# Optimization experiments

Hardware: AMD Instinct MI355X
Metric: run time of the kernel (lower is better)

## Reference

```python
import jax, jax.numpy as jnp
import numpy as np

TOP_K = 2
INIT_STD = 0.02
B, T, D, E, I = 2, 2048, 1024, 8, 512


def setup_inputs() -> dict:
    key = jax.random.key(0)
    k0, k1, k2, k3, k4 = jax.random.split(key, 5)
    return {
        "x": jax.random.normal(k0, (B, T, D), dtype=jnp.float32),
        "router_w": (jax.random.normal(k1, (E, D), dtype=jnp.float32) * INIT_STD),
        "w_gate": (jax.random.normal(k2, (E, I, D), dtype=jnp.float32) * INIT_STD),
        "w_up": (jax.random.normal(k3, (E, I, D), dtype=jnp.float32) * INIT_STD),
        "w_down": (jax.random.normal(k4, (E, D, I), dtype=jnp.float32) * INIT_STD),
    }


def _moe_forward(x, router_w, w_gate, w_up, w_down):
    # x: [B, T, D]; router_w: [E, D]; w_gate/w_up: [E, I, D]; w_down: [E, D, I]
    b, t, d = x.shape
    e = router_w.shape[0]
    gate_logits = jnp.einsum('btd,ed->bte', x, router_w)          # [B, T, E]
    top_w, sel = jax.lax.top_k(gate_logits, TOP_K)                # [B, T, K]
    probs = jax.nn.softmax(top_w, axis=-1)                        # softmax over selected experts only

    n = b * t
    xf = x.reshape(n, d)                                          # [N, D]
    sel_f = sel.reshape(n, TOP_K)
    probs_f = probs.reshape(n, TOP_K)
    # combine weights per (token, expert); zero for unselected experts
    gates = jnp.zeros((n, e), dtype=x.dtype).at[
        jnp.arange(n)[:, None], sel_f].add(probs_f)               # [N, E]

    # SwiGLU expert FFN (no bias). Gated-dense formulation: unselected experts
    # have gate weight exactly 0, so this is bit-for-bit the same math as
    # dispatch + grouped GEMM + combine. scan over experts keeps memory at
    # one [N, I] intermediate at a time.
    def body(acc, ws):
        wg, wu, wd, g = ws                                        # [I,D],[I,D],[D,I],[N]
        h = jax.nn.silu(xf @ wg.T) * (xf @ wu.T)                  # [N, I]
        return acc + g[:, None] * (h @ wd.T), None

    out, _ = jax.lax.scan(body, jnp.zeros((n, d), dtype=x.dtype),
                          (w_gate, w_up, w_down, gates.T))
    return out.reshape(b, t, d), gate_logits


def reference(x, router_w, w_gate, w_up, w_down):
    return _moe_forward(x, router_w, w_gate, w_up, w_down)
```

## Files before the change

### kernel.cpp

```cpp
#include <hip/hip_runtime.h>
#include <cstdint>

#define N_TOK 4096
#define D_    1024
#define E_    8
#define I_    512
#define KTOP  2
#define PAD   64
#define BK    64
#define CAP   (N_TOK*KTOP + E_*PAD)
#define NBX   (CAP / PAD)
#define WSZ   ((size_t)E_ * I_ * D_)

typedef __attribute__((ext_vector_type(4))) float f32x4;
typedef __attribute__((ext_vector_type(8))) short bf16x8;

__device__ inline unsigned short f2bf(float f) {
  union { float f; uint32_t u; } v; v.f = f;
  uint32_t r = v.u + 0x7fffu + ((v.u >> 16) & 1u);
  return (unsigned short)(r >> 16);
}
__device__ inline float bf2f(unsigned short h) {
  union { uint32_t u; float f; } v; v.u = ((uint32_t)h) << 16;
  return v.f;
}

#define GLOAD_LDS16(gp, lp)                                                        \
  __builtin_amdgcn_global_load_lds((const __attribute__((address_space(1))) void*)(gp), \
                                   (__attribute__((address_space(3))) void*)(lp), 16, 0, 0)

__global__ __launch_bounds__(256) void convertw_kernel(const float* __restrict__ wg,
                                                       const float* __restrict__ wu,
                                                       const float* __restrict__ wd,
                                                       unsigned short* __restrict__ dst) {
  const int y = blockIdx.y;
  const float* s = (y == 0) ? wg : (y == 1) ? wu : wd;
  unsigned short* d = dst + (size_t)y * WSZ;
  int i = blockIdx.x * 256 + threadIdx.x;
  const float4 v = reinterpret_cast<const float4*>(s)[i];
  ushort4 o;
  o.x = f2bf(v.x); o.y = f2bf(v.y); o.z = f2bf(v.z); o.w = f2bf(v.w);
  reinterpret_cast<ushort4*>(d)[i] = o;
}

__global__ __launch_bounds__(256) void router_kernel(const float* __restrict__ x,
                                                     const float* __restrict__ rw,
                                                     float* __restrict__ logits,
                                                     int* __restrict__ sel,
                                                     float* __restrict__ prob,
                                                     unsigned short* __restrict__ Xb) {
  const int lane = threadIdx.x & 63;
  const int tok  = blockIdx.x * 4 + (threadIdx.x >> 6);
  const float4* xr = reinterpret_cast<const float4*>(x + (size_t)tok * D_);
  float4 xv[4];
#pragma unroll
  for (int q = 0; q < 4; ++q) xv[q] = xr[q * 64 + lane];
  float acc[E_];
#pragma unroll
  for (int e = 0; e < E_; ++e) {
    const float4* wr = reinterpret_cast<const float4*>(rw + (size_t)e * D_);
    float s = 0.f;
#pragma unroll
    for (int q = 0; q < 4; ++q) {
      float4 wv = wr[q * 64 + lane];
      s += xv[q].x * wv.x + xv[q].y * wv.y + xv[q].z * wv.z + xv[q].w * wv.w;
    }
    acc[e] = s;
  }
  ushort4* xb = reinterpret_cast<ushort4*>(Xb + (size_t)tok * D_);
#pragma unroll
  for (int q = 0; q < 4; ++q) {
    ushort4 o;
    o.x = f2bf(xv[q].x); o.y = f2bf(xv[q].y); o.z = f2bf(xv[q].z); o.w = f2bf(xv[q].w);
    xb[q * 64 + lane] = o;
  }
#pragma unroll
  for (int e = 0; e < E_; ++e)
#pragma unroll
    for (int off = 32; off; off >>= 1) acc[e] += __shfl_xor(acc[e], off);
  if (lane == 0) {
    float v0 = -1e30f, v1 = -1e30f; int i0 = 0, i1 = 0;
#pragma unroll
    for (int e = 0; e < E_; ++e) {
      float v = acc[e];
      logits[(size_t)tok * E_ + e] = v;
      if (v > v0)      { v1 = v0; i1 = i0; v0 = v; i0 = e; }
      else if (v > v1) { v1 = v;  i1 = e; }
    }
    float t  = __expf(v1 - v0);
    sel[tok * 2] = i0; sel[tok * 2 + 1] = i1;
    prob[tok * 2] = 1.f / (1.f + t);
    prob[tok * 2 + 1] = t / (1.f + t);
  }
}

__global__ __launch_bounds__(1024) void plan_kernel(const int* __restrict__ sel,
                                                    const float* __restrict__ prob,
                                                    int* __restrict__ offs,
                                                    int* __restrict__ ptok,
                                                    float* __restrict__ pprob,
                                                    int* __restrict__ tpos,
                                                    unsigned int* __restrict__ zbuf) {
  __shared__ int wcnt[16][E_];
  __shared__ int pfx[16][E_];
  __shared__ int soffs[E_ + 1];
  __shared__ int secnt[E_];
  const int tid = threadIdx.x;
  const int wave = tid >> 6, lane = tid & 63;
  const unsigned long long lt = (1ull << lane) - 1ull;

  zbuf[tid] = 0u;

  int   mye[8];
  int   mylp[8];
  float myp[8];
  int run[E_];
#pragma unroll
  for (int e = 0; e < E_; ++e) run[e] = 0;

#pragma unroll
  for (int it = 0; it < 8; ++it) {
    int i = wave * 512 + it * 64 + lane;
    int e = sel[i];
    mye[it] = e;
    myp[it] = prob[i];
    int lp = 0;
#pragma unroll
    for (int ee = 0; ee < E_; ++ee) {
      unsigned long long m = __ballot(e == ee);
      if (e == ee) lp = run[ee] + __popcll(m & lt);
      run[ee] += __popcll(m);
    }
    mylp[it] = lp;
  }
#pragma unroll
  for (int ee = 0; ee < E_; ++ee)
    if (lane == ee) wcnt[wave][ee] = run[ee];
  __syncthreads();

  if (tid == 0) {
    int ro = 0;
#pragma unroll
    for (int e = 0; e < E_; ++e) {
      int c = 0;
      int r = ro;
      for (int w = 0; w < 16; ++w) { pfx[w][e] = r; r += wcnt[w][e]; c += wcnt[w][e]; }
      soffs[e] = ro; offs[e] = ro; secnt[e] = c;
      ro += (c + PAD - 1) & ~(PAD - 1);
    }
    soffs[E_] = ro; offs[E_] = ro;
  }
  __syncthreads();

#pragma unroll
  for (int it = 0; it < 8; ++it) {
    int i = wave * 512 + it * 64 + lane;
    int pos = pfx[wave][mye[it]] + mylp[it];
    ptok[pos]  = i >> 1;
    pprob[pos] = myp[it];
    tpos[i]    = pos;
  }
#pragma unroll
  for (int e = 0; e < E_; ++e) {
    int s = soffs[e] + secnt[e];
    int npad = soffs[e + 1] - s;
    if (tid < npad) { ptok[s + tid] = -1; pprob[s + tid] = 0.f; }
  }
}

__global__ __launch_bounds__(256, 4) void gemm1_kernel(const unsigned short* __restrict__ Xb,
                                                       const unsigned short* __restrict__ Wg,
                                                       const unsigned short* __restrict__ Wu,
                                                       const int* __restrict__ ptok,
                                                       const int* __restrict__ offs,
                                                       const unsigned short* __restrict__ zbuf,
                                                       unsigned short* __restrict__ H) {
  __shared__ unsigned short As[PAD * BK];
  __shared__ unsigned short Bg[64 * BK];
  __shared__ unsigned short Bu[64 * BK];
  __shared__ int toks[PAD];

  const int wgid = (blockIdx.x & 7) * 136 + (blockIdx.x >> 3);
  const int bx = wgid >> 3;
  const int by = wgid & 7;

  const int total = offs[E_];
  const int t0 = bx * PAD;
  if (t0 >= total) return;
  int e = 0;
#pragma unroll
  for (int i = 1; i < E_; ++i) if (offs[i] <= t0) e = i;

  const int tid  = threadIdx.x;
  const int lane = tid & 63;
  const int w    = tid >> 6;
  if (tid < PAD) toks[tid] = ptok[t0 + tid];
  __syncthreads();

  const int ib    = by * 64;
  const int gcol8 = (lane & 7) ^ (lane >> 3);

  const unsigned short* asrc[2];
  const unsigned short* bgsrc[2];
  const unsigned short* busrc[2];
#pragma unroll
  for (int i = 0; i < 2; ++i) {
    int r = w * 16 + i * 8 + (lane >> 3);
    int t = toks[r];
    asrc[i] = (t >= 0) ? (Xb + (size_t)t * D_ + gcol8 * 8) : (zbuf + gcol8 * 8);
    size_t rowoff = ((size_t)e * I_ + ib + r) * D_ + gcol8 * 8;
    bgsrc[i] = Wg + rowoff;
    busrc[i] = Wu + rowoff;
  }

  f32x4 accg[2][2], accu[2][2];
#pragma unroll
  for (int m = 0; m < 2; ++m)
#pragma unroll
    for (int n = 0; n < 2; ++n) {
      accg[m][n] = (f32x4){0.f, 0.f, 0.f, 0.f};
      accu[m][n] = (f32x4){0.f, 0.f, 0.f, 0.f};
    }

  const int wr = w >> 1, wc = w & 1;
  const int xr7 = lane & 7;

  for (int k0 = 0; k0 < D_; k0 += BK) {
#pragma unroll
    for (int i = 0; i < 2; ++i) {
      GLOAD_LDS16(asrc[i] + k0, &As[(w * 2 + i) * 512]);
      GLOAD_LDS16(bgsrc[i] + k0, &Bg[(w * 2 + i) * 512]);
      GLOAD_LDS16(busrc[i] + k0, &Bu[(w * 2 + i) * 512]);
    }
    __syncthreads();
#pragma unroll
    for (int kk = 0; kk < 2; ++kk) {
      const int uoff = ((kk * 4 + (lane >> 4)) ^ xr7) * 8;
      bf16x8 a[2], bg[2], bu[2];
#pragma unroll
      for (int m = 0; m < 2; ++m) {
        int row = wr * 32 + m * 16 + (lane & 15);
        a[m] = *reinterpret_cast<const bf16x8*>(&As[row * BK + uoff]);
      }
#pragma unroll
      for (int n = 0; n < 2; ++n) {
        int row = wc * 32 + n * 16 + (lane & 15);
        bg[n] = *reinterpret_cast<const bf16x8*>(&Bg[row * BK + uoff]);
        bu[n] = *reinterpret_cast<const bf16x8*>(&Bu[row * BK + uoff]);
      }
#pragma unroll
      for (int m = 0; m < 2; ++m)
#pragma unroll
        for (int n = 0; n < 2; ++n) {
          accg[m][n] = __builtin_amdgcn_mfma_f32_16x16x32_bf16(bg[n], a[m], accg[m][n], 0, 0, 0);
          accu[m][n] = __builtin_amdgcn_mfma_f32_16x16x32_bf16(bu[n], a[m], accu[m][n], 0, 0, 0);
        }
    }
    __syncthreads();
  }

#pragma unroll
  for (int m = 0; m < 2; ++m) {
    const int trow = wr * 32 + m * 16 + (lane & 15);
#pragma unroll
    for (int n = 0; n < 2; ++n) {
      const int icb = ib + wc * 32 + n * 16 + (lane >> 4) * 4;
      ushort4 st;
      float g, uu, h;
      g = accg[m][n][0]; uu = accu[m][n][0]; h = (g / (1.f + __expf(-g))) * uu; st.x = f2bf(h);
      g = accg[m][n][1]; uu = accu[m][n][1]; h = (g / (1.f + __expf(-g))) * uu; st.y = f2bf(h);
      g = accg[m][n][2]; uu = accu[m][n][2]; h = (g / (1.f + __expf(-g))) * uu; st.z = f2bf(h);
      g = accg[m][n][3]; uu = accu[m][n][3]; h = (g / (1.f + __expf(-g))) * uu; st.w = f2bf(h);
      *reinterpret_cast<ushort4*>(&H[(size_t)(t0 + trow) * I_ + icb]) = st;
    }
  }
}

__global__ __launch_bounds__(256, 4) void gemm2_kernel(const unsigned short* __restrict__ H,
                                                       const unsigned short* __restrict__ Wd,
                                                       const float* __restrict__ pprob,
                                                       const int* __restrict__ offs,
                                                       unsigned short* __restrict__ O) {
  __shared__ unsigned short As[PAD * BK];
  __shared__ unsigned short Bs[128 * BK];
  __shared__ float probs[PAD];

  const int wgid = (blockIdx.x & 7) * 136 + (blockIdx.x >> 3);
  const int bx = wgid >> 3;
  const int by = wgid & 7;

  const int total = offs[E_];
  const int t0 = bx * PAD;
  if (t0 >= total) return;
  int e = 0;
#pragma unroll
  for (int i = 1; i < E_; ++i) if (offs[i] <= t0) e = i;

  const int tid  = threadIdx.x;
  const int lane = tid & 63;
  const int w    = tid >> 6;
  if (tid < PAD) probs[tid] = pprob[t0 + tid];
  __syncthreads();

  const int db    = by * 128;
  const int gcol8 = (lane & 7) ^ (lane >> 3);

  const unsigned short* asrc[2];
#pragma unroll
  for (int i = 0; i < 2; ++i) {
    int r = w * 16 + i * 8 + (lane >> 3);
    asrc[i] = H + (size_t)(t0 + r) * I_ + gcol8 * 8;
  }
  const unsigned short* bsrc[4];
#pragma unroll
  for (int i = 0; i < 4; ++i) {
    int r = w * 32 + i * 8 + (lane >> 3);
    bsrc[i] = Wd + ((size_t)e * D_ + db + r) * I_ + gcol8 * 8;
  }

  f32x4 acc[2][4];
#pragma unroll
  for (int m = 0; m < 2; ++m)
#pragma unroll
    for (int n = 0; n < 4; ++n) acc[m][n] = (f32x4){0.f, 0.f, 0.f, 0.f};

  const int wr = w >> 1, wc = w & 1;
  const int xr7 = lane & 7;

  for (int k0 = 0; k0 < I_; k0 += BK) {
#pragma unroll
    for (int i = 0; i < 2; ++i) GLOAD_LDS16(asrc[i] + k0, &As[(w * 2 + i) * 512]);
#pragma unroll
    for (int i = 0; i < 4; ++i) GLOAD_LDS16(bsrc[i] + k0, &Bs[(w * 4 + i) * 512]);
    __syncthreads();
#pragma unroll
    for (int kk = 0; kk < 2; ++kk) {
      const int uoff = ((kk * 4 + (lane >> 4)) ^ xr7) * 8;
      bf16x8 a[2], b[4];
#pragma unroll
      for (int m = 0; m < 2; ++m) {
        int row = wr * 32 + m * 16 + (lane & 15);
        a[m] = *reinterpret_cast<const bf16x8*>(&As[row * BK + uoff]);
      }
#pragma unroll
      for (int n = 0; n < 4; ++n) {
        int row = wc * 64 + n * 16 + (lane & 15);
        b[n] = *reinterpret_cast<const bf16x8*>(&Bs[row * BK + uoff]);
      }
#pragma unroll
      for (int m = 0; m < 2; ++m)
#pragma unroll
        for (int n = 0; n < 4; ++n)
          acc[m][n] = __builtin_amdgcn_mfma_f32_16x16x32_bf16(b[n], a[m], acc[m][n], 0, 0, 0);
    }
    __syncthreads();
  }

#pragma unroll
  for (int m = 0; m < 2; ++m) {
    const int trow = wr * 32 + m * 16 + (lane & 15);
    const float p = probs[trow];
#pragma unroll
    for (int n = 0; n < 4; ++n) {
      const int dcb = db + wc * 64 + n * 16 + (lane >> 4) * 4;
      ushort4 v;
      v.x = f2bf(acc[m][n][0] * p); v.y = f2bf(acc[m][n][1] * p);
      v.z = f2bf(acc[m][n][2] * p); v.w = f2bf(acc[m][n][3] * p);
      *reinterpret_cast<ushort4*>(&O[(size_t)(t0 + trow) * D_ + dcb]) = v;
    }
  }
}

__global__ __launch_bounds__(256) void combine_kernel(const unsigned short* __restrict__ O,
                                                      const int* __restrict__ tpos,
                                                      float* __restrict__ out) {
  const int t = blockIdx.x;
  const int c = threadIdx.x;
  const int p0 = tpos[2 * t], p1 = tpos[2 * t + 1];
  const ushort4 a = reinterpret_cast<const ushort4*>(O + (size_t)p0 * D_)[c];
  const ushort4 b = reinterpret_cast<const ushort4*>(O + (size_t)p1 * D_)[c];
  float4 r;
  r.x = bf2f(a.x) + bf2f(b.x); r.y = bf2f(a.y) + bf2f(b.y);
  r.z = bf2f(a.z) + bf2f(b.z); r.w = bf2f(a.w) + bf2f(b.w);
  reinterpret_cast<float4*>(out + (size_t)t * D_)[c] = r;
}

extern "C" void kernel_launch(void* const* d_in, const int* in_sizes, int n_in,
                              void* d_out, int out_size, void* d_ws, size_t ws_size,
                              hipStream_t stream) {
  const float* x  = (const float*)d_in[0];
  const float* rw = (const float*)d_in[1];
  const float* wg = (const float*)d_in[2];
  const float* wu = (const float*)d_in[3];
  const float* wd = (const float*)d_in[4];
  float* out    = (float*)d_out;
  float* logits = out + (size_t)N_TOK * D_;

  char* ws = (char*)d_ws;
  int*   offs  = (int*)(ws + 64);
  unsigned short* zbuf = (unsigned short*)(ws + 256);
  int*   sel   = (int*)  (ws + 4352);
  float* prob  = (float*)(ws + 37120);
  int*   ptok  = (int*)  (ws + 69888);
  float* pprob = (float*)(ws + 104704);
  int*   tpos  = (int*)  (ws + 139520);
  unsigned short* Xb  = (unsigned short*)(ws + 172288);
  unsigned short* Wgb = Xb  + (size_t)N_TOK * D_;
  unsigned short* Wub = Wgb + WSZ;
  unsigned short* Wdb = Wub + WSZ;
  unsigned short* Hb  = Wdb + WSZ;
  unsigned short* Opos = Hb + (size_t)CAP * I_;

  convertw_kernel<<<dim3(WSZ / 4 / 256, 3), 256, 0, stream>>>(wg, wu, wd, Wgb);
  router_kernel<<<N_TOK / 4, 256, 0, stream>>>(x, rw, logits, sel, prob, Xb);
  plan_kernel<<<1, 1024, 0, stream>>>(sel, prob, offs, ptok, pprob, tpos, (unsigned int*)zbuf);
  gemm1_kernel<<<NBX * 8, 256, 0, stream>>>(Xb, Wgb, Wub, ptok, offs, zbuf, Hb);
  gemm2_kernel<<<NBX * 8, 256, 0, stream>>>(Hb, Wdb, pprob, offs, Opos);
  combine_kernel<<<N_TOK, 256, 0, stream>>>(Opos, tpos, out);
}
```

Baseline: 91.62 us.

## Switch GEMMs to 32x32x16 MFMA, merge weight-convert and router kernels, drop zero buffer

```diff
diff --git a/kernel.cpp b/kernel.cpp
--- a/kernel.cpp
+++ b/kernel.cpp
@@ -12,8 +12,8 @@
 #define NBX   (CAP / PAD)
 #define WSZ   ((size_t)E_ * I_ * D_)
 
-typedef __attribute__((ext_vector_type(4))) float f32x4;
-typedef __attribute__((ext_vector_type(8))) short bf16x8;
+typedef __attribute__((ext_vector_type(16))) float f32x16;
+typedef __attribute__((ext_vector_type(8)))  short bf16x8;
 
 __device__ inline unsigned short f2bf(float f) {
   union { float f; uint32_t u; } v; v.f = f;
@@ -29,28 +29,31 @@
   __builtin_amdgcn_global_load_lds((const __attribute__((address_space(1))) void*)(gp), \
                                    (__attribute__((address_space(3))) void*)(lp), 16, 0, 0)
 
-__global__ __launch_bounds__(256) void convertw_kernel(const float* __restrict__ wg,
-                                                       const float* __restrict__ wu,
-                                                       const float* __restrict__ wd,
-                                                       unsigned short* __restrict__ dst) {
-  const int y = blockIdx.y;
-  const float* s = (y == 0) ? wg : (y == 1) ? wu : wd;
-  unsigned short* d = dst + (size_t)y * WSZ;
-  int i = blockIdx.x * 256 + threadIdx.x;
-  const float4 v = reinterpret_cast<const float4*>(s)[i];
-  ushort4 o;
-  o.x = f2bf(v.x); o.y = f2bf(v.y); o.z = f2bf(v.z); o.w = f2bf(v.w);
-  reinterpret_cast<ushort4*>(d)[i] = o;
-}
-
-__global__ __launch_bounds__(256) void router_kernel(const float* __restrict__ x,
-                                                     const float* __restrict__ rw,
-                                                     float* __restrict__ logits,
-                                                     int* __restrict__ sel,
-                                                     float* __restrict__ prob,
-                                                     unsigned short* __restrict__ Xb) {
+__global__ __launch_bounds__(256) void prep_kernel(const float* __restrict__ x,
+                                                   const float* __restrict__ rw,
+                                                   const float* __restrict__ wg,
+                                                   const float* __restrict__ wu,
+                                                   const float* __restrict__ wd,
+                                                   float* __restrict__ logits,
+                                                   int* __restrict__ sel,
+                                                   float* __restrict__ prob,
+                                                   unsigned short* __restrict__ Xb,
+                                                   unsigned short* __restrict__ Wb) {
+  int b = blockIdx.x;
+  if (b < 3 * 4096) {
+    const int y = b >> 12;
+    const float* s = (y == 0) ? wg : (y == 1) ? wu : wd;
+    unsigned short* d = Wb + (size_t)y * WSZ;
+    const int i = (b & 4095) * 256 + threadIdx.x;
+    const float4 v = reinterpret_cast<const float4*>(s)[i];
+    ushort4 o;
+    o.x = f2bf(v.x); o.y = f2bf(v.y); o.z = f2bf(v.z); o.w = f2bf(v.w);
+    reinterpret_cast<ushort4*>(d)[i] = o;
+    return;
+  }
+  b -= 3 * 4096;
   const int lane = threadIdx.x & 63;
-  const int tok  = blockIdx.x * 4 + (threadIdx.x >> 6);
+  const int tok  = b * 4 + (threadIdx.x >> 6);
   const float4* xr = reinterpret_cast<const float4*>(x + (size_t)tok * D_);
   float4 xv[4];
 #pragma unroll
@@ -99,8 +102,7 @@
                                                     int* __restrict__ offs,
                                                     int* __restrict__ ptok,
                                                     float* __restrict__ pprob,
-                                                    int* __restrict__ tpos,
-                                                    unsigned int* __restrict__ zbuf) {
+                                                    int* __restrict__ tpos) {
   __shared__ int wcnt[16][E_];
   __shared__ int pfx[16][E_];
   __shared__ int soffs[E_ + 1];
@@ -109,8 +111,6 @@
   const int wave = tid >> 6, lane = tid & 63;
   const unsigned long long lt = (1ull << lane) - 1ull;
 
-  zbuf[tid] = 0u;
-
   int   mye[8];
   int   mylp[8];
   float myp[8];
@@ -164,7 +164,7 @@
   for (int e = 0; e < E_; ++e) {
     int s = soffs[e] + secnt[e];
     int npad = soffs[e + 1] - s;
-    if (tid < npad) { ptok[s + tid] = -1; pprob[s + tid] = 0.f; }
+    if (tid < npad) { ptok[s + tid] = 0; pprob[s + tid] = 0.f; }
   }
 }
 
@@ -173,7 +173,6 @@
                                                        const unsigned short* __restrict__ Wu,
                                                        const int* __restrict__ ptok,
                                                        const int* __restrict__ offs,
-                                                       const unsigned short* __restrict__ zbuf,
                                                        unsigned short* __restrict__ H) {
   __shared__ unsigned short As[PAD * BK];
   __shared__ unsigned short Bg[64 * BK];
@@ -206,24 +205,20 @@
 #pragma unroll
   for (int i = 0; i < 2; ++i) {
     int r = w * 16 + i * 8 + (lane >> 3);
-    int t = toks[r];
-    asrc[i] = (t >= 0) ? (Xb + (size_t)t * D_ + gcol8 * 8) : (zbuf + gcol8 * 8);
+    asrc[i] = Xb + (size_t)toks[r] * D_ + gcol8 * 8;
     size_t rowoff = ((size_t)e * I_ + ib + r) * D_ + gcol8 * 8;
     bgsrc[i] = Wg + rowoff;
     busrc[i] = Wu + rowoff;
   }
 
-  f32x4 accg[2][2], accu[2][2];
-#pragma unroll
-  for (int m = 0; m < 2; ++m)
-#pragma unroll
-    for (int n = 0; n < 2; ++n) {
-      accg[m][n] = (f32x4){0.f, 0.f, 0.f, 0.f};
-      accu[m][n] = (f32x4){0.f, 0.f, 0.f, 0.f};
-    }
+  f32x16 accg = {0.f}, accu = {0.f};
+#pragma unroll
+  for (int j = 0; j < 16; ++j) { accg[j] = 0.f; accu[j] = 0.f; }
 
   const int wr = w >> 1, wc = w & 1;
   const int xr7 = lane & 7;
+  const int arow = wr * 32 + (lane & 31);
+  const int brow = wc * 32 + (lane & 31);
 
   for (int k0 = 0; k0 < D_; k0 += BK) {
 #pragma unroll
@@ -234,45 +229,28 @@
     }
     __syncthreads();
 #pragma unroll
-    for (int kk = 0; kk < 2; ++kk) {
-      const int uoff = ((kk * 4 + (lane >> 4)) ^ xr7) * 8;
-      bf16x8 a[2], bg[2], bu[2];
-#pragma unroll
-      for (int m = 0; m < 2; ++m) {
-        int row = wr * 32 + m * 16 + (lane & 15);
-        a[m] = *reinterpret_cast<const bf16x8*>(&As[row * BK + uoff]);
-      }
-#pragma unroll
-      for (int n = 0; n < 2; ++n) {
-        int row = wc * 32 + n * 16 + (lane & 15);
-        bg[n] = *reinterpret_cast<const bf16x8*>(&Bg[row * BK + uoff]);
-        bu[n] = *reinterpret_cast<const bf16x8*>(&Bu[row * BK + uoff]);
-      }
-#pragma unroll
-      for (int m = 0; m < 2; ++m)
-#pragma unroll
-        for (int n = 0; n < 2; ++n) {
-          accg[m][n] = __builtin_amdgcn_mfma_f32_16x16x32_bf16(bg[n], a[m], accg[m][n], 0, 0, 0);
-          accu[m][n] = __builtin_amdgcn_mfma_f32_16x16x32_bf16(bu[n], a[m], accu[m][n], 0, 0, 0);
-        }
+    for (int sk = 0; sk < 4; ++sk) {
+      const int uoff = ((sk * 2 + (lane >> 5)) ^ xr7) * 8;
+      bf16x8 a  = *reinterpret_cast<const bf16x8*>(&As[arow * BK + uoff]);
+      bf16x8 bg = *reinterpret_cast<const bf16x8*>(&Bg[brow * BK + uoff]);
+      bf16x8 bu = *reinterpret_cast<const bf16x8*>(&Bu[brow * BK + uoff]);
+      accg = __builtin_amdgcn_mfma_f32_32x32x16_bf16(bg, a, accg, 0, 0, 0);
+      accu = __builtin_amdgcn_mfma_f32_32x32x16_bf16(bu, a, accu, 0, 0, 0);
     }
     __syncthreads();
   }
 
-#pragma unroll
-  for (int m = 0; m < 2; ++m) {
-    const int trow = wr * 32 + m * 16 + (lane & 15);
-#pragma unroll
-    for (int n = 0; n < 2; ++n) {
-      const int icb = ib + wc * 32 + n * 16 + (lane >> 4) * 4;
-      ushort4 st;
-      float g, uu, h;
-      g = accg[m][n][0]; uu = accu[m][n][0]; h = (g / (1.f + __expf(-g))) * uu; st.x = f2bf(h);
-      g = accg[m][n][1]; uu = accu[m][n][1]; h = (g / (1.f + __expf(-g))) * uu; st.y = f2bf(h);
-      g = accg[m][n][2]; uu = accu[m][n][2]; h = (g / (1.f + __expf(-g))) * uu; st.z = f2bf(h);
-      g = accg[m][n][3]; uu = accu[m][n][3]; h = (g / (1.f + __expf(-g))) * uu; st.w = f2bf(h);
-      *reinterpret_cast<ushort4*>(&H[(size_t)(t0 + trow) * I_ + icb]) = st;
-    }
+  const int hrow = t0 + wr * 32 + (lane & 31);
+#pragma unroll
+  for (int q = 0; q < 4; ++q) {
+    const int icb = ib + wc * 32 + q * 8 + (lane >> 5) * 4;
+    ushort4 st;
+    float g, uu, h;
+    g = accg[q*4+0]; uu = accu[q*4+0]; h = (g / (1.f + __expf(-g))) * uu; st.x = f2bf(h);
+    g = accg[q*4+1]; uu = accu[q*4+1]; h = (g / (1.f + __expf(-g))) * uu; st.y = f2bf(h);
+    g = accg[q*4+2]; uu = accu[q*4+2]; h = (g / (1.f + __expf(-g))) * uu; st.z = f2bf(h);
+    g = accg[q*4+3]; uu = accu[q*4+3]; h = (g / (1.f + __expf(-g))) * uu; st.w = f2bf(h);
+    *reinterpret_cast<ushort4*>(&H[(size_t)hrow * I_ + icb]) = st;
   }
 }
 
@@ -318,14 +296,15 @@
     bsrc[i] = Wd + ((size_t)e * D_ + db + r) * I_ + gcol8 * 8;
   }
 
-  f32x4 acc[2][4];
-#pragma unroll
-  for (int m = 0; m < 2; ++m)
-#pragma unroll
-    for (int n = 0; n < 4; ++n) acc[m][n] = (f32x4){0.f, 0.f, 0.f, 0.f};
+  f32x16 acc0 = {0.f}, acc1 = {0.f};
+#pragma unroll
+  for (int j = 0; j < 16; ++j) { acc0[j] = 0.f; acc1[j] = 0.f; }
 
   const int wr = w >> 1, wc = w & 1;
   const int xr7 = lane & 7;
+  const int arow  = wr * 32 + (lane & 31);
+  const int brow0 = wc * 64 + (lane & 31);
+  const int brow1 = wc * 64 + 32 + (lane & 31);
 
   for (int k0 = 0; k0 < I_; k0 += BK) {
 #pragma unroll
@@ -334,40 +313,31 @@
     for (int i = 0; i < 4; ++i) GLOAD_LDS16(bsrc[i] + k0, &Bs[(w * 4 + i) * 512]);
     __syncthreads();
 #pragma unroll
-    for (int kk = 0; kk < 2; ++kk) {
-      const int uoff = ((kk * 4 + (lane >> 4)) ^ xr7) * 8;
-      bf16x8 a[2], b[4];
-#pragma unroll
-      for (int m = 0; m < 2; ++m) {
-        int row = wr * 32 + m * 16 + (lane & 15);
-        a[m] = *reinterpret_cast<const bf16x8*>(&As[row * BK + uoff]);
-      }
-#pragma unroll
-      for (int n = 0; n < 4; ++n) {
-        int row = wc * 64 + n * 16 + (lane & 15);
-        b[n] = *reinterpret_cast<const bf16x8*>(&Bs[row * BK + uoff]);
-      }
-#pragma unroll
-      for (int m = 0; m < 2; ++m)
-#pragma unroll
-        for (int n = 0; n < 4; ++n)
-          acc[m][n] = __builtin_amdgcn_mfma_f32_16x16x32_bf16(b[n], a[m], acc[m][n], 0, 0, 0);
+    for (int sk = 0; sk < 4; ++sk) {
+      const int uoff = ((sk * 2 + (lane >> 5)) ^ xr7) * 8;
+      bf16x8 a  = *reinterpret_cast<const bf16x8*>(&As[arow * BK + uoff]);
+      bf16x8 b0 = *reinterpret_cast<const bf16x8*>(&Bs[brow0 * BK + uoff]);
+      bf16x8 b1 = *reinterpret_cast<const bf16x8*>(&Bs[brow1 * BK + uoff]);
+      acc0 = __builtin_amdgcn_mfma_f32_32x32x16_bf16(b0, a, acc0, 0, 0, 0);
+      acc1 = __builtin_amdgcn_mfma_f32_32x32x16_bf16(b1, a, acc1, 0, 0, 0);
     }
     __syncthreads();
   }
 
-#pragma unroll
-  for (int m = 0; m < 2; ++m) {
-    const int trow = wr * 32 + m * 16 + (lane & 15);
-    const float p = probs[trow];
-#pragma unroll
-    for (int n = 0; n < 4; ++n) {
-      const int dcb = db + wc * 64 + n * 16 + (lane >> 4) * 4;
-      ushort4 v;
-      v.x = f2bf(acc[m][n][0] * p); v.y = f2bf(acc[m][n][1] * p);
-      v.z = f2bf(acc[m][n][2] * p); v.w = f2bf(acc[m][n][3] * p);
-      *reinterpret_cast<ushort4*>(&O[(size_t)(t0 + trow) * D_ + dcb]) = v;
-    }
+  const int prow = wr * 32 + (lane & 31);
+  const float p = probs[prow];
+  const int orow = t0 + prow;
+#pragma unroll
+  for (int q = 0; q < 4; ++q) {
+    const int dcb0 = db + wc * 64 + q * 8 + (lane >> 5) * 4;
+    ushort4 v;
+    v.x = f2bf(acc0[q*4+0] * p); v.y = f2bf(acc0[q*4+1] * p);
+    v.z = f2bf(acc0[q*4+2] * p); v.w = f2bf(acc0[q*4+3] * p);
+    *reinterpret_cast<ushort4*>(&O[(size_t)orow * D_ + dcb0]) = v;
+    ushort4 v1;
+    v1.x = f2bf(acc1[q*4+0] * p); v1.y = f2bf(acc1[q*4+1] * p);
+    v1.z = f2bf(acc1[q*4+2] * p); v1.w = f2bf(acc1[q*4+3] * p);
+    *reinterpret_cast<ushort4*>(&O[(size_t)orow * D_ + dcb0 + 32]) = v1;
   }
 }
 
@@ -398,7 +368,6 @@
 
   char* ws = (char*)d_ws;
   int*   offs  = (int*)(ws + 64);
-  unsigned short* zbuf = (unsigned short*)(ws + 256);
   int*   sel   = (int*)  (ws + 4352);
   float* prob  = (float*)(ws + 37120);
   int*   ptok  = (int*)  (ws + 69888);
@@ -411,10 +380,10 @@
   unsigned short* Hb  = Wdb + WSZ;
   unsigned short* Opos = Hb + (size_t)CAP * I_;
 
-  convertw_kernel<<<dim3(WSZ / 4 / 256, 3), 256, 0, stream>>>(wg, wu, wd, Wgb);
-  router_kernel<<<N_TOK / 4, 256, 0, stream>>>(x, rw, logits, sel, prob, Xb);
-  plan_kernel<<<1, 1024, 0, stream>>>(sel, prob, offs, ptok, pprob, tpos, (unsigned int*)zbuf);
-  gemm1_kernel<<<NBX * 8, 256, 0, stream>>>(Xb, Wgb, Wub, ptok, offs, zbuf, Hb);
+  prep_kernel<<<3 * 4096 + N_TOK / 4, 256, 0, stream>>>(x, rw, wg, wu, wd,
+                                                        logits, sel, prob, Xb, Wgb);
+  plan_kernel<<<1, 1024, 0, stream>>>(sel, prob, offs, ptok, pprob, tpos);
+  gemm1_kernel<<<NBX * 8, 256, 0, stream>>>(Xb, Wgb, Wub, ptok, offs, Hb);
   gemm2_kernel<<<NBX * 8, 256, 0, stream>>>(Hb, Wdb, pprob, offs, Opos);
   combine_kernel<<<N_TOK, 256, 0, stream>>>(Opos, tpos, out);
 }
```

Measured after the change: 91.75 us. About the same (+0.1%).
